# Performance work log

Hardware: AMD Instinct MI355X
Metric: run time of the kernel (lower is better)

Reference implementation:

```python
import jax, jax.numpy as jnp
import numpy as np

B, LQ, LK = 4, 128, 1024
Q_SIZE, K_SIZE, V_SIZE, UNITS = 512, 512, 512, 256
MASK_VAL = -1e6  # matches torch masked_softmax value=-1000000.0


def setup_inputs() -> dict:
    key = jax.random.key(0)
    ks = jax.random.split(key, 7)
    return {
        "query": jax.random.normal(ks[0], (B, LQ, Q_SIZE), dtype=jnp.float32),
        "key": jax.random.normal(ks[1], (B, LK, K_SIZE), dtype=jnp.float32),
        "value": jax.random.normal(ks[2], (B, LK, V_SIZE), dtype=jnp.float32),
        "valid_len": jax.random.randint(ks[3], (B,), 1, LK + 1).astype(jnp.int64),
        # torch nn.Linear(in, out, bias=False) weight is (out, in)
        "W_q": jax.random.normal(ks[4], (UNITS, Q_SIZE), dtype=jnp.float32) / np.sqrt(Q_SIZE),
        "W_k": jax.random.normal(ks[5], (UNITS, K_SIZE), dtype=jnp.float32) / np.sqrt(K_SIZE),
        "v": jax.random.normal(ks[6], (UNITS,), dtype=jnp.float32) / np.sqrt(UNITS),
    }


def reference(query, key, value, valid_len, W_q, W_k, v):
    # projections: (B,Lq,units), (B,Lk,units)
    q = jnp.einsum("bqd,ud->bqu", query, W_q)
    k = jnp.einsum("bkd,ud->bku", key, W_k)
    # additive features: (B,Lq,Lk,units)
    feats = jnp.tanh(q[:, :, None, :] + k[:, None, :, :])
    # v-projection -> scores (B,Lq,Lk)
    scores = jnp.einsum("bqku,u->bqk", feats, v)
    # mask positions >= valid_len with -1e6 (same as torch sequence_mask)
    mask = jnp.arange(scores.shape[-1]) < valid_len[:, None, None]
    scores = jnp.where(mask, scores, MASK_VAL)
    attn = jax.nn.softmax(scores, axis=-1)  # dropout rate is 0.0
    return jnp.einsum("bqk,bkv->bqv", attn, value)
```

## Files before the change

### kernel.cpp

```cpp
#include <hip/hip_runtime.h>


typedef _Float16 half8 __attribute__((ext_vector_type(8)));
typedef float floatx4 __attribute__((ext_vector_type(4)));

#define EQ_OFF   0
#define EKT_OFF  (512 * 256)

__global__ __launch_bounds__(256) void proj_mfma(
    const float* __restrict__ query, const float* __restrict__ key,
    const float* __restrict__ W_q, const float* __restrict__ W_k,
    const int* __restrict__ vlen, float* __restrict__ Eq,
    float* __restrict__ EkT) {
  __shared__ __align__(16) _Float16 As[64 * 32];
  __shared__ __align__(16) _Float16 Bs[64 * 32];
  const int tid = threadIdx.x;
  const int mb = blockIdx.x;
  const int u0 = blockIdx.y * 64;
  const bool qpart = mb < 8;
  const float *Ag, *Bg;
  int kbatch = 0, j0 = 0, m0 = 0;
  if (qpart) {
    m0 = mb * 64;
    Ag = query + (size_t)m0 * 512;
    Bg = W_q + (size_t)u0 * 512;
  } else {
    const int g0 = (mb - 8) * 64;
    kbatch = g0 >> 10;
    j0 = g0 & 1023;
    if (j0 >= vlen[kbatch]) return;
    Ag = W_k + (size_t)u0 * 512;
    Bg = key + (size_t)g0 * 512;
  }

  const int lrow = tid >> 2, lkq = (tid & 3) * 8;
  const float* Ags = Ag + lrow * 512 + lkq;
  const float* Bgs = Bg + lrow * 512 + lkq;
  _Float16* Ads = As + lrow * 32 + lkq;
  _Float16* Bds = Bs + lrow * 32 + lkq;

  const int lane = tid & 63;
  const int wid = tid >> 6;
  const int wm = (wid & 1) * 32, wn = (wid >> 1) * 32;
  const int frow = lane & 15;
  const int fk = (lane >> 4) * 8;

  floatx4 acc[2][2] = {{{0.f, 0.f, 0.f, 0.f}, {0.f, 0.f, 0.f, 0.f}},
                       {{0.f, 0.f, 0.f, 0.f}, {0.f, 0.f, 0.f, 0.f}}};

  float4 ra0 = *(const float4*)Ags;
  float4 ra1 = *(const float4*)(Ags + 4);
  float4 rb0 = *(const float4*)Bgs;
  float4 rb1 = *(const float4*)(Bgs + 4);

  for (int kb = 0; kb < 16; ++kb) {
    half8 ha, hb;
    ha[0] = (_Float16)ra0.x; ha[1] = (_Float16)ra0.y;
    ha[2] = (_Float16)ra0.z; ha[3] = (_Float16)ra0.w;
    ha[4] = (_Float16)ra1.x; ha[5] = (_Float16)ra1.y;
    ha[6] = (_Float16)ra1.z; ha[7] = (_Float16)ra1.w;
    hb[0] = (_Float16)rb0.x; hb[1] = (_Float16)rb0.y;
    hb[2] = (_Float16)rb0.z; hb[3] = (_Float16)rb0.w;
    hb[4] = (_Float16)rb1.x; hb[5] = (_Float16)rb1.y;
    hb[6] = (_Float16)rb1.z; hb[7] = (_Float16)rb1.w;
    __syncthreads();
    *(half8*)Ads = ha;
    *(half8*)Bds = hb;
    __syncthreads();
    if (kb + 1 < 16) {
      ra0 = *(const float4*)(Ags + (kb + 1) * 32);
      ra1 = *(const float4*)(Ags + (kb + 1) * 32 + 4);
      rb0 = *(const float4*)(Bgs + (kb + 1) * 32);
      rb1 = *(const float4*)(Bgs + (kb + 1) * 32 + 4);
    }
    half8 a0 = *(const half8*)(As + (wm + frow) * 32 + fk);
    half8 a1 = *(const half8*)(As + (wm + 16 + frow) * 32 + fk);
    half8 b0 = *(const half8*)(Bs + (wn + frow) * 32 + fk);
    half8 b1 = *(const half8*)(Bs + (wn + 16 + frow) * 32 + fk);
    acc[0][0] = __builtin_amdgcn_mfma_f32_16x16x32_f16(a0, b0, acc[0][0], 0, 0, 0);
    acc[0][1] = __builtin_amdgcn_mfma_f32_16x16x32_f16(a0, b1, acc[0][1], 0, 0, 0);
    acc[1][0] = __builtin_amdgcn_mfma_f32_16x16x32_f16(a1, b0, acc[1][0], 0, 0, 0);
    acc[1][1] = __builtin_amdgcn_mfma_f32_16x16x32_f16(a1, b1, acc[1][1], 0, 0, 0);
  }

  const int rbase = (lane >> 4) * 4;
  const int col = lane & 15;
#pragma unroll
  for (int mi = 0; mi < 2; ++mi)
#pragma unroll
    for (int ni = 0; ni < 2; ++ni)
#pragma unroll
      for (int r = 0; r < 4; ++r) {
        const int R = wm + mi * 16 + rbase + r;
        const int C = wn + ni * 16 + col;
        const float e = __expf(2.f * acc[mi][ni][r]);
        if (qpart)
          Eq[(m0 + R) * 256 + u0 + C] = e;
        else
          EkT[kbatch * 262144 + (u0 + R) * 1024 + j0 + C] = e;
      }
}

__global__ __launch_bounds__(1024) void scores_attn(
    const float* __restrict__ Eq, const float* __restrict__ EkT,
    const float* __restrict__ vvec, const int* __restrict__ valid_len,
    const float* __restrict__ value, float* __restrict__ out) {
  __shared__ float4 QV[256];
  __shared__ float P0[1024];
  __shared__ float P1[1024];
  __shared__ float2 red[16];
  const int tid = threadIdx.x;
  const int b = blockIdx.x >> 6;
  const int i0 = (blockIdx.x & 63) * 2;
  const int vl = valid_len[b];

  if (tid < 256) {
    float vv = vvec[tid];
    QV[tid] = make_float4(Eq[(b * 128 + i0) * 256 + tid],
                          Eq[(b * 128 + i0 + 1) * 256 + tid], -2.f * vv, vv);
  }
  __syncthreads();

  const int j = tid;
  float p0 = 0.f, p1 = 0.f;
  if (j < vl) {
    float a0 = 0.f, a1 = 0.f, sv = 0.f;
    const float* kp = EkT + b * 262144 + j;
#pragma unroll 8
    for (int u = 0; u < 256; ++u) {
      float ek = kp[u << 10];
      float4 q = QV[u];
      sv += q.w;
      float r0 = __builtin_amdgcn_rcpf(fmaf(q.x, ek, 1.f));
      float r1 = __builtin_amdgcn_rcpf(fmaf(q.y, ek, 1.f));
      a0 = fmaf(q.z, r0, a0);
      a1 = fmaf(q.z, r1, a1);
    }
    p0 = __expf(sv + a0);
    p1 = __expf(sv + a1);
  }
  P0[j] = p0;
  P1[j] = p1;

  float2 pp = make_float2(p0, p1);
#pragma unroll
  for (int off = 32; off > 0; off >>= 1) {
    pp.x += __shfl_xor(pp.x, off, 64);
    pp.y += __shfl_xor(pp.y, off, 64);
  }
  if ((tid & 63) == 0) red[tid >> 6] = pp;
  __syncthreads();
  float den0 = 0.f, den1 = 0.f;
#pragma unroll
  for (int w = 0; w < 16; ++w) { den0 += red[w].x; den1 += red[w].y; }

  const int r = tid >> 9;
  const int c = tid & 511;
  const float* P = r ? P1 : P0;
  const float* Vb = value + b * 524288 + c;
  float acc0 = 0.f, acc1 = 0.f;
  int jj = 0;
  for (; jj + 8 <= vl; jj += 8) {
#pragma unroll
    for (int t = 0; t < 8; t += 2) {
      acc0 = fmaf(P[jj + t], Vb[(jj + t) * 512], acc0);
      acc1 = fmaf(P[jj + t + 1], Vb[(jj + t + 1) * 512], acc1);
    }
  }
  for (; jj < vl; ++jj) acc0 = fmaf(P[jj], Vb[jj * 512], acc0);
  const float rden = __builtin_amdgcn_rcpf(r ? den1 : den0);
  out[(b * 128 + i0 + r) * 512 + c] = (acc0 + acc1) * rden;
}

extern "C" void kernel_launch(void* const* d_in, const int* in_sizes, int n_in,
                              void* d_out, int out_size, void* d_ws, size_t ws_size,
                              hipStream_t stream) {
  const float* query = (const float*)d_in[0];
  const float* key   = (const float*)d_in[1];
  const float* value = (const float*)d_in[2];
  const int*   vlen  = (const int*)d_in[3];
  const float* W_q   = (const float*)d_in[4];
  const float* W_k   = (const float*)d_in[5];
  const float* v     = (const float*)d_in[6];
  float* out = (float*)d_out;

  float* ws  = (float*)d_ws;
  float* Eq  = ws + EQ_OFF;
  float* EkT = ws + EKT_OFF;

  proj_mfma<<<dim3(72, 4), 256, 0, stream>>>(query, key, W_q, W_k, vlen, Eq, EkT);
  scores_attn<<<256, 1024, 0, stream>>>(Eq, EkT, v, vlen, value, out);
}
```

Before: 129.3 us.

## Split PV product across key chunks with float4 loads and shared reduction

After: 113.5 us, median of 2. 12.2% less time.

```diff
diff --git a/kernel.cpp b/kernel.cpp
--- a/kernel.cpp
+++ b/kernel.cpp
@@ -109,35 +109,43 @@
   __shared__ float P0[1024];
   __shared__ float P1[1024];
   __shared__ float2 red[16];
+  __shared__ float4 red2[8][2][128];
   const int tid = threadIdx.x;
   const int b = blockIdx.x >> 6;
   const int i0 = (blockIdx.x & 63) * 2;
   const int vl = valid_len[b];
 
+  float vv = 0.f;
   if (tid < 256) {
-    float vv = vvec[tid];
+    vv = vvec[tid];
     QV[tid] = make_float4(Eq[(b * 128 + i0) * 256 + tid],
-                          Eq[(b * 128 + i0 + 1) * 256 + tid], -2.f * vv, vv);
-  }
-  __syncthreads();
+                          Eq[(b * 128 + i0 + 1) * 256 + tid], -2.f * vv, 0.f);
+  }
+  float sv = vv;
+#pragma unroll
+  for (int off = 32; off > 0; off >>= 1) sv += __shfl_xor(sv, off, 64);
+  if ((tid & 63) == 0) red[tid >> 6] = make_float2(sv, 0.f);
+  __syncthreads();
+  float SV = 0.f;
+#pragma unroll
+  for (int w = 0; w < 16; ++w) SV += red[w].x;
 
   const int j = tid;
   float p0 = 0.f, p1 = 0.f;
   if (j < vl) {
-    float a0 = 0.f, a1 = 0.f, sv = 0.f;
+    float a0 = 0.f, a1 = 0.f;
     const float* kp = EkT + b * 262144 + j;
 #pragma unroll 8
     for (int u = 0; u < 256; ++u) {
       float ek = kp[u << 10];
       float4 q = QV[u];
-      sv += q.w;
       float r0 = __builtin_amdgcn_rcpf(fmaf(q.x, ek, 1.f));
       float r1 = __builtin_amdgcn_rcpf(fmaf(q.y, ek, 1.f));
       a0 = fmaf(q.z, r0, a0);
       a1 = fmaf(q.z, r1, a1);
     }
-    p0 = __expf(sv + a0);
-    p1 = __expf(sv + a1);
+    p0 = __expf(SV + a0);
+    p1 = __expf(SV + a1);
   }
   P0[j] = p0;
   P1[j] = p1;
@@ -148,28 +156,50 @@
     pp.x += __shfl_xor(pp.x, off, 64);
     pp.y += __shfl_xor(pp.y, off, 64);
   }
+  __syncthreads();
   if ((tid & 63) == 0) red[tid >> 6] = pp;
   __syncthreads();
   float den0 = 0.f, den1 = 0.f;
 #pragma unroll
   for (int w = 0; w < 16; ++w) { den0 += red[w].x; den1 += red[w].y; }
 
-  const int r = tid >> 9;
-  const int c = tid & 511;
-  const float* P = r ? P1 : P0;
-  const float* Vb = value + b * 524288 + c;
-  float acc0 = 0.f, acc1 = 0.f;
-  int jj = 0;
-  for (; jj + 8 <= vl; jj += 8) {
-#pragma unroll
-    for (int t = 0; t < 8; t += 2) {
-      acc0 = fmaf(P[jj + t], Vb[(jj + t) * 512], acc0);
-      acc1 = fmaf(P[jj + t + 1], Vb[(jj + t + 1) * 512], acc1);
-    }
-  }
-  for (; jj < vl; ++jj) acc0 = fmaf(P[jj], Vb[jj * 512], acc0);
-  const float rden = __builtin_amdgcn_rcpf(r ? den1 : den0);
-  out[(b * 128 + i0 + r) * 512 + c] = (acc0 + acc1) * rden;
+  const int cg = tid & 127;
+  const int jq = tid >> 7;
+  const float* Vb = value + b * 524288 + cg * 4;
+  float4 acc0 = make_float4(0.f, 0.f, 0.f, 0.f);
+  float4 acc1 = make_float4(0.f, 0.f, 0.f, 0.f);
+  const int js = jq * 128;
+  const int je = min(js + 128, vl);
+  for (int j4 = js; j4 < je; j4 += 4) {
+    float4 q0 = *(const float4*)(P0 + j4);
+    float4 q1 = *(const float4*)(P1 + j4);
+#pragma unroll
+    for (int t = 0; t < 4; ++t) {
+      float4 v4 = *(const float4*)(Vb + (j4 + t) * 512);
+      float w0 = t == 0 ? q0.x : t == 1 ? q0.y : t == 2 ? q0.z : q0.w;
+      float w1 = t == 0 ? q1.x : t == 1 ? q1.y : t == 2 ? q1.z : q1.w;
+      acc0.x = fmaf(w0, v4.x, acc0.x); acc0.y = fmaf(w0, v4.y, acc0.y);
+      acc0.z = fmaf(w0, v4.z, acc0.z); acc0.w = fmaf(w0, v4.w, acc0.w);
+      acc1.x = fmaf(w1, v4.x, acc1.x); acc1.y = fmaf(w1, v4.y, acc1.y);
+      acc1.z = fmaf(w1, v4.z, acc1.z); acc1.w = fmaf(w1, v4.w, acc1.w);
+    }
+  }
+  red2[jq][0][cg] = acc0;
+  red2[jq][1][cg] = acc1;
+  __syncthreads();
+
+  if (tid < 256) {
+    const int r = tid >> 7, cg2 = tid & 127;
+    float4 s = make_float4(0.f, 0.f, 0.f, 0.f);
+#pragma unroll
+    for (int q = 0; q < 8; ++q) {
+      float4 x = red2[q][r][cg2];
+      s.x += x.x; s.y += x.y; s.z += x.z; s.w += x.w;
+    }
+    const float rden = __builtin_amdgcn_rcpf(r ? den1 : den0);
+    s.x *= rden; s.y *= rden; s.z *= rden; s.w *= rden;
+    *(float4*)(out + (b * 128 + i0 + r) * 512 + cg2 * 4) = s;
+  }
 }
 
 extern "C" void kernel_launch(void* const* d_in, const int* in_sizes, int n_in,
```
